# Kernel tuning notes

Measured on AMD Instinct MI355X. Metric: run time of the kernel, lower is better.

## Reference

```python
import jax, jax.numpy as jnp
import numpy as np

E = 1024   # embed_dim
H = 16     # num_heads
HD = E // H
T, B, S = 1024, 4, 1024


def setup_inputs() -> dict:
    key = jax.random.key(0)
    ks = jax.random.split(key, 6)
    g = lambda k, sh, sc=1.0: jax.random.normal(k, sh, dtype=jnp.float32) * sc
    return {
        "query": g(ks[0], (T, B, E)),
        "key": g(ks[1], (S, B, E)),
        "value": g(ks[2], (S, B, E)),
        "in_proj_weight": g(ks[3], (3 * E, E), E ** -0.5),
        "in_proj_bias": jnp.zeros((3 * E,), jnp.float32),
        "out_w": g(ks[4], (E, E), E ** -0.5),
        "out_b": jnp.zeros((E,), jnp.float32),
    }


def reference(query, key, value, in_proj_weight, in_proj_bias, out_w, out_b):
    # qkv not same and kv not same -> decorr=True cross-attention branch.
    W, b = in_proj_weight, in_proj_bias
    scaling = HD ** -0.5
    half = E // 2
    # Note: original uses F.linear(x, weight_slice.T, bias) == x @ weight_slice + bias
    q = query @ W[:E] + b[:E]                       # [T,B,E]
    k = key @ W[E:2 * E] + b[E:2 * E]               # [S,B,E]
    Wv = W[2 * E:]                                  # [E,E] V block
    v_corr = value @ Wv[:, :half] + b[2 * E:2 * E + half]      # [S,B,E/2]
    v_decorr = value @ Wv[:, half:] + b[2 * E + half:]         # [S,B,E/2]
    q = q * scaling
    # heads: [T,B,E] -> [B*H, T, hd]; per-branch V has head_dim/2 per head
    qh = q.reshape(T, B * H, HD).transpose(1, 0, 2)
    kh = k.reshape(S, B * H, HD).transpose(1, 0, 2)
    vch = v_corr.reshape(S, B * H, HD // 2).transpose(1, 0, 2)
    vdh = v_decorr.reshape(S, B * H, HD // 2).transpose(1, 0, 2)
    scores = jnp.einsum('btd,bsd->bts', qh, kh)     # [B*H, T, S]
    a_corr = jax.nn.softmax(scores, axis=-1)
    a_decorr = jax.nn.softmax(-scores, axis=-1)     # softmin(x) = softmax(-x)
    # dropout p=0.0 (eval) -> identity
    attn = jnp.concatenate([
        jnp.einsum('bts,bsd->btd', a_corr, vch),
        jnp.einsum('bts,bsd->btd', a_decorr, vdh),
    ], axis=-1)                                     # [B*H, T, HD]
    attn = attn.transpose(1, 0, 2).reshape(T, B, E)
    attn = attn @ out_w.T + out_b                   # nn.Linear out_proj
    # returned attn_weights are the RAW (pre-softmax) scores averaged over heads
    avg_w = scores.reshape(B, H, T, S).sum(axis=1) / H
    return attn, avg_w
```

## Files before the change

kernel.cpp:

```cpp
#include <hip/hip_runtime.h>
#include <hip/hip_bf16.h>


typedef __bf16 bf16;
typedef float f32x4 __attribute__((ext_vector_type(4)));
typedef float float4v __attribute__((ext_vector_type(4)));
typedef bf16 bf16x8 __attribute__((ext_vector_type(8)));
typedef bf16 bf16x4 __attribute__((ext_vector_type(4)));

#define LOG2E 1.4426950408889634f

__device__ __forceinline__ void gll16(const void* g, void* l) {
  __builtin_amdgcn_global_load_lds(
      (const __attribute__((address_space(1))) void*)g,
      (__attribute__((address_space(3))) void*)l, 16, 0, 0);
}

__device__ __forceinline__ int xcd_swz(int flat, int nwg) {
  int q = nwg >> 3;
  return (flat & 7) * q + (flat >> 3);
}

__device__ __forceinline__ bf16x4 cvt4(float4v v) {
  bf16x4 b = { (bf16)v.x, (bf16)v.y, (bf16)v.z, (bf16)v.w };
  return b;
}

__global__ __launch_bounds__(256) void prep_all(
    const float* __restrict__ W, const float* __restrict__ out_w,
    bf16* __restrict__ WT, bf16* __restrict__ owb) {
  __shared__ bf16 tile[64][72];
  int bid = blockIdx.x;
  if (bid >= 768) {
    int i = ((bid - 768) * 256 + (int)threadIdx.x) * 4;
    float4v v = *(const float4v*)(out_w + i);
    *(bf16x4*)&owb[i] = cvt4(v);
    return;
  }
  int sec = bid >> 8, bx = bid & 15, by = (bid >> 4) & 15;
  int i0 = by * 64, j0 = bx * 64;
  const float* s = W + (long)sec * 1048576;
  bf16* d = WT + (long)sec * 1048576;
  int t = threadIdx.x;
#pragma unroll
  for (int p = 0; p < 4; p++) {
    int ri = (t >> 4) + p * 16, cj = (t & 15) * 4;
    float4v vv = *(const float4v*)(s + (long)(i0 + ri) * 1024 + j0 + cj);
    *(bf16x4*)&tile[ri][cj] = cvt4(vv);
  }
  __syncthreads();
#pragma unroll
  for (int p = 0; p < 4; p++) {
    int rj = (t >> 4) + p * 16, ci = (t & 15) * 4;
    bf16x4 bv = { tile[ci][rj], tile[ci + 1][rj], tile[ci + 2][rj], tile[ci + 3][rj] };
    *(bf16x4*)&d[(long)(j0 + rj) * 1024 + i0 + ci] = bv;
  }
}

template <bool AF32>
__device__ __forceinline__ void gemm_core(
    const void* __restrict__ Av, long lda,
    const bf16* __restrict__ B, long ldb,
    void* __restrict__ C, long ldc,
    const float* __restrict__ bias, float scale, int K,
    int m0, int n0, int cmode) {
  __shared__ bf16 smem[AF32 ? 24576 : 16384];
  float* sAf = (float*)smem;
  bf16* sBb = smem + (AF32 ? 16384 : 8192);
  int t = threadIdx.x;
  int w = t >> 6, lane = t & 63, r = lane & 15, g = lane >> 4;
  int mq = (w >> 1) * 32, nq = (w & 1) * 64;
  int srow = w * 16 + (lane >> 2);
  int scol = ((lane & 3) ^ ((srow >> 1) & 3)) * 8;
  int fsw = (r >> 1) & 3;
  const bf16* Bs = B + (long)(n0 + srow) * ldb + scol;
  const bf16* As = (const bf16*)Av + (long)(m0 + srow) * lda + scol;
  int aro = lane >> 3;
  int acolf = 4 * ((lane & 7) ^ aro);
  const float* Af = (const float*)Av + (long)(m0 + w * 16 + aro) * lda + acolf;

  f32x4 acc[2][4];
#pragma unroll
  for (int mi = 0; mi < 2; mi++)
#pragma unroll
    for (int ni = 0; ni < 4; ni++) acc[mi][ni] = (f32x4){0.f, 0.f, 0.f, 0.f};

  auto stage = [&](int buf, int k) {
    if (AF32) {
      gll16(Af + k, sAf + buf * 4096 + w * 512);
      gll16(Af + 8 * lda + k, sAf + buf * 4096 + w * 512 + 256);
    } else {
      gll16(As + k, &smem[buf * 4096 + w * 512]);
    }
    gll16(Bs + k, &sBb[buf * 4096 + w * 512]);
  };
  stage(0, 0);
  __syncthreads();
  int cur = 0;
  for (int k0 = 0; k0 < K; k0 += 32) {
    if (k0 + 32 < K) stage(cur ^ 1, k0 + 32);
    bf16x8 af[2], bfr[4];
    if (AF32) {
      int rk = r & 7;
#pragma unroll
      for (int mi = 0; mi < 2; mi++) {
        int row = mq + mi * 16 + r;
        const float* pa = sAf + cur * 4096 + row * 32;
        float4v lo = *(const float4v*)(pa + 4 * ((2 * g) ^ rk));
        float4v hi = *(const float4v*)(pa + 4 * ((2 * g + 1) ^ rk));
        bf16x4 l4 = cvt4(lo), h4 = cvt4(hi);
        bf16x8 a = { l4[0], l4[1], l4[2], l4[3], h4[0], h4[1], h4[2], h4[3] };
        af[mi] = a;
      }
    } else {
#pragma unroll
      for (int mi = 0; mi < 2; mi++)
        af[mi] = *(bf16x8*)&smem[cur * 4096 + (mq + mi * 16 + r) * 32 + 8 * (g ^ fsw)];
    }
#pragma unroll
    for (int ni = 0; ni < 4; ni++)
      bfr[ni] = *(bf16x8*)&sBb[cur * 4096 + (nq + ni * 16 + r) * 32 + 8 * (g ^ fsw)];
#pragma unroll
    for (int mi = 0; mi < 2; mi++)
#pragma unroll
      for (int ni = 0; ni < 4; ni++)
        acc[mi][ni] = __builtin_amdgcn_mfma_f32_16x16x32_bf16(af[mi], bfr[ni], acc[mi][ni], 0, 0, 0);
    __syncthreads();
    cur ^= 1;
  }

  if (cmode == 2) {
#pragma unroll
    for (int mi = 0; mi < 2; mi++) {
      int tl = (mq >> 2) + mi * 4 + g;
#pragma unroll
      for (int ni = 0; ni < 4; ni++) {
        int cl = nq + ni * 16 + r;
        float bv = bias ? bias[n0 + cl] : 0.f;
        int chunkb = (nq >> 6) * 2560 + tl * 80 + ni * 16 + r;
#pragma unroll
        for (int j = 0; j < 4; j++) {
          float val = (acc[mi][ni][j] + bv) * scale;
          smem[j * 5120 + chunkb] = (bf16)val;
        }
      }
    }
    __syncthreads();
    {
      int b_ = w >> 1, hl = w & 1;
      long gbase = ((long)(b_ * 16 + (n0 >> 6) + hl)) * 65536 + (long)(m0 >> 2) * 64;
#pragma unroll
      for (int it = 0; it < 4; it++) {
        bf16x8 v = *(bf16x8*)&smem[w * 2560 + (it * 8 + (lane >> 3)) * 80 + (lane & 7) * 8];
        *(bf16x8*)&((bf16*)C)[gbase + it * 512 + lane * 8] = v;
      }
    }
    return;
  }

  if (cmode == 3) {
#pragma unroll
    for (int mi = 0; mi < 2; mi++) {
      int s32 = (mq >> 2) + mi * 4 + g;
      int gq = (s32 >> 2) & 3;
      int u = ((s32 >> 4) << 2) | (s32 & 3);
#pragma unroll
      for (int ni = 0; ni < 4; ni++) {
        int col = n0 + nq + ni * 16 + r;
        float bv = bias ? bias[col] : 0.f;
        int clbase = ((nq >> 5) + (ni >> 1)) * 2 + (ni & 1);
#pragma unroll
        for (int j = 0; j < 4; j++) {
          float val = (acc[mi][ni][j] + bv) * scale;
          smem[(j * 8 + clbase) * 512 + (gq * 16 + r) * 8 + u] = (bf16)val;
        }
      }
    }
    __syncthreads();
    int sc_ = m0 >> 7;
    int hh0 = (n0 & 511) >> 5;
    int half = n0 >> 9;
#pragma unroll
    for (int c = 0; c < 4; c++) {
      int cl = w * 4 + c;
      int b_ = cl >> 3, hl = (cl >> 1) & 3, dl = cl & 1;
      long chunk = ((long)(b_ * 16 + hh0 + hl) * 32 + sc_) * 4 + half * 2 + dl;
      bf16x8 v = *(bf16x8*)&smem[cl * 512 + lane * 8];
      *(bf16x8*)&((bf16*)C)[(chunk << 9) + lane * 8] = v;
    }
    return;
  }

#pragma unroll
  for (int mi = 0; mi < 2; mi++)
#pragma unroll
    for (int ni = 0; ni < 4; ni++) {
      int col = n0 + nq + ni * 16 + r;
      float bv = bias ? bias[col] : 0.f;
#pragma unroll
      for (int j = 0; j < 4; j++) {
        int row = m0 + mq + mi * 16 + g * 4 + j;
        float val = (acc[mi][ni][j] + bv) * scale;
        if (cmode == 1) {
          ((bf16*)C)[(long)row * ldc + col] = (bf16)val;
        } else {
          ((float*)C)[(long)row * ldc + col] = val;
        }
      }
    }
}

__global__ __launch_bounds__(512) void gemm_out(
    const bf16* __restrict__ A, const bf16* __restrict__ B,
    float* __restrict__ C, const float* __restrict__ bias) {
  int nwg = gridDim.x * gridDim.y;
  int flat = blockIdx.x + gridDim.x * blockIdx.y;
  int work = xcd_swz(flat, nwg);
  int n = work % gridDim.x, m = work / gridDim.x;
  gemm_core<false>(A, 1024, B, 1024, C, 1024, bias, 1.0f, 1024, m * 128, n * 128, 0);
}

__global__ __launch_bounds__(512) void gemm_proj(
    const float* __restrict__ q, const float* __restrict__ k,
    const float* __restrict__ v, const bf16* __restrict__ WT,
    const float* __restrict__ bias, bf16* __restrict__ qkout,
    bf16* __restrict__ vf) {
  int nwg = gridDim.x * gridDim.y * gridDim.z;
  int flat = blockIdx.x + gridDim.x * (blockIdx.y + gridDim.y * blockIdx.z);
  int work = xcd_swz(flat, nwg);
  int n = work % gridDim.x;
  int m = (work / gridDim.x) % gridDim.y;
  int z = work / (gridDim.x * gridDim.y);
  const float* A = (z == 0) ? q : ((z == 1) ? k : v);
  const bf16* B = WT + (long)z * 1048576;
  const float* bz = bias + z * 1024;
  void* C = (z == 2) ? (void*)vf : (void*)(qkout + (long)z * 4194304);
  float scale = (z == 0) ? 0.125f * LOG2E : 1.0f;
  gemm_core<true>(A, 1024, B, 1024, C, 1024, bz, scale, 1024, m * 128, n * 128,
                  z == 2 ? 3 : 2);
}

__global__ __launch_bounds__(512) void attn_avg(
    const bf16* __restrict__ qh, const bf16* __restrict__ kh,
    const bf16* __restrict__ vf, bf16* __restrict__ attn_b,
    float* __restrict__ out_avg, float avg_scale) {
  __shared__ __align__(16) bf16 smem[16384];
  int tid = threadIdx.x, w = tid >> 6, lane = tid & 63, r = lane & 15, g = lane >> 4;
  int fsw = (r >> 1) & 3;

  if (blockIdx.x >= 512) {
    bf16* sA = smem;
    bf16* sB = smem + 8192;
    int work = xcd_swz(blockIdx.x - 512, 256);
    int n0 = (work & 7) * 128;
    int m0 = ((work >> 3) & 7) * 128;
    int bb = work >> 6;
    int mq = (w >> 1) * 32, nq = (w & 1) * 64;
    int srow = w * 16 + (lane >> 2);
    int scol = ((lane & 3) ^ ((srow >> 1) & 3)) * 8;
    const bf16* As = qh + (long)bb * 1048576 + (long)(m0 + srow) * 64 + scol;
    const bf16* Bs = kh + (long)bb * 1048576 + (long)(n0 + srow) * 64 + scol;

    f32x4 acc[2][4];
#pragma unroll
    for (int mi = 0; mi < 2; mi++)
#pragma unroll
      for (int ni = 0; ni < 4; ni++) acc[mi][ni] = (f32x4){0.f, 0.f, 0.f, 0.f};

    gll16(As, &sA[w * 512]);
    gll16(Bs, &sB[w * 512]);
    __syncthreads();
    int cur = 0;
    for (int k0 = 0; k0 < 1024; k0 += 32) {
      if (k0 + 32 < 1024) {
        int kn = k0 + 32;
        long off = ((long)(kn >> 6)) * 65536 + (kn & 63);
        gll16(As + off, &sA[(cur ^ 1) * 4096 + w * 512]);
        gll16(Bs + off, &sB[(cur ^ 1) * 4096 + w * 512]);
      }
      bf16x8 af[2], bfr[4];
#pragma unroll
      for (int mi = 0; mi < 2; mi++)
        af[mi] = *(bf16x8*)&sA[cur * 4096 + (mq + mi * 16 + r) * 32 + 8 * (g ^ fsw)];
#pragma unroll
      for (int ni = 0; ni < 4; ni++)
        bfr[ni] = *(bf16x8*)&sB[cur * 4096 + (nq + ni * 16 + r) * 32 + 8 * (g ^ fsw)];
#pragma unroll
      for (int mi = 0; mi < 2; mi++)
#pragma unroll
        for (int ni = 0; ni < 4; ni++)
          acc[mi][ni] = __builtin_amdgcn_mfma_f32_16x16x32_bf16(af[mi], bfr[ni], acc[mi][ni], 0, 0, 0);
      __syncthreads();
      cur ^= 1;
    }
#pragma unroll
    for (int mi = 0; mi < 2; mi++)
#pragma unroll
      for (int ni = 0; ni < 4; ni++) {
        int col = n0 + nq + ni * 16 + r;
#pragma unroll
        for (int j = 0; j < 4; j++) {
          int row = m0 + mq + mi * 16 + g * 4 + j;
          out_avg[(long)bb * 1048576 + (long)row * 1024 + col] = acc[mi][ni][j] * avg_scale;
        }
      }
    return;
  }

  bf16* sK = smem;
  bf16* sV = smem + 8192;
  int bh = blockIdx.x & 63;
  int b = bh >> 4, h = bh & 15;
  int t0 = (blockIdx.x >> 6) * 128;
  int tw = t0 + w * 16;

  const bf16* qrow = qh + ((long)bh * 1024 + tw + r) * 64;
  bf16x8 aq0 = *(const bf16x8*)(qrow + g * 8);
  bf16x8 aq1 = *(const bf16x8*)(qrow + 32 + g * 8);

  float sp_acc = 0.f, sn_acc = 0.f;
  f32x4 o[4];
#pragma unroll
  for (int d = 0; d < 4; d++) o[d] = (f32x4){0.f, 0.f, 0.f, 0.f};

  const bf16* kbh = kh + (long)bh * 65536;
  const bf16* vbh = vf + (long)bh * 65536;

  int krow = w * 8 + (lane >> 3);
  const bf16* ksrc = kbh + (long)krow * 64 + 8 * ((lane & 7) ^ (krow & 7));
  const bf16* vsrc = vbh + w * 512 + lane * 8;
  int c0 = 8 * (g ^ (r & 7));
  int c1 = 8 * ((g + 4) ^ (r & 7));

  gll16(ksrc, &sK[w * 512]);
  gll16(vsrc, &sV[w * 512]);
  __syncthreads();
  int cur = 0;
#pragma unroll 1
  for (int st = 0; st < 16; st++) {
    if (st < 15) {
      gll16(ksrc + (st + 1) * 4096, &sK[(cur ^ 1) * 4096 + w * 512]);
      gll16(vsrc + (st + 1) * 4096, &sV[(cur ^ 1) * 4096 + w * 512]);
    }
    f32x4 sc4[4];
#pragma unroll
    for (int sf = 0; sf < 4; sf++) {
      int row = sf * 16 + r;
      bf16x8 k0 = *(const bf16x8*)&sK[cur * 4096 + row * 64 + c0];
      bf16x8 k1 = *(const bf16x8*)&sK[cur * 4096 + row * 64 + c1];
      f32x4 z = (f32x4){0.f, 0.f, 0.f, 0.f};
      z = __builtin_amdgcn_mfma_f32_16x16x32_bf16(k0, aq0, z, 0, 0, 0);
      z = __builtin_amdgcn_mfma_f32_16x16x32_bf16(k1, aq1, z, 0, 0, 0);
      sc4[sf] = z;
    }
    bf16x8 pP[2], pN[2];
#pragma unroll
    for (int sf = 0; sf < 4; sf++)
#pragma unroll
      for (int j = 0; j < 4; j++) {
        float e = __builtin_amdgcn_exp2f(sc4[sf][j]);
        sp_acc += e;
        pP[sf >> 1][(sf & 1) * 4 + j] = (bf16)e;
        float f = __builtin_amdgcn_exp2f(-sc4[sf][j]);
        sn_acc += f;
        pN[sf >> 1][(sf & 1) * 4 + j] = (bf16)f;
      }
#pragma unroll
    for (int c = 0; c < 2; c++)
#pragma unroll
      for (int dblk = 0; dblk < 4; dblk++) {
        bf16x8 vv = *(const bf16x8*)&sV[cur * 4096 + (c * 4 + dblk) * 512 + lane * 8];
        o[dblk] = __builtin_amdgcn_mfma_f32_16x16x32_bf16(
            vv, (dblk < 2) ? pP[c] : pN[c], o[dblk], 0, 0, 0);
      }
    __syncthreads();
    cur ^= 1;
  }

  sp_acc += __shfl_xor(sp_acc, 16); sp_acc += __shfl_xor(sp_acc, 32);
  sn_acc += __shfl_xor(sn_acc, 16); sn_acc += __shfl_xor(sn_acc, 32);
  float rlp = 1.f / sp_acc, rln = 1.f / sn_acc;
  long obase = ((long)(tw + r) * 4 + b) * 1024 + h * 64;
#pragma unroll
  for (int dblk = 0; dblk < 4; dblk++) {
    float rl = (dblk < 2) ? rlp : rln;
    bf16x4 ov;
#pragma unroll
    for (int j = 0; j < 4; j++) ov[j] = (bf16)(o[dblk][j] * rl);
    *(bf16x4*)&attn_b[obase + (dblk >> 1) * 32 + (dblk & 1) * 16 + g * 4] = ov;
  }
}

extern "C" void kernel_launch(void* const* d_in, const int* in_sizes, int n_in,
                              void* d_out, int out_size, void* d_ws, size_t ws_size,
                              hipStream_t stream) {
  (void)in_sizes; (void)n_in; (void)out_size; (void)ws_size;
  const float* query = (const float*)d_in[0];
  const float* key   = (const float*)d_in[1];
  const float* value = (const float*)d_in[2];
  const float* W     = (const float*)d_in[3];
  const float* bias  = (const float*)d_in[4];
  const float* out_w = (const float*)d_in[5];
  const float* out_b = (const float*)d_in[6];

  char* ws = (char*)d_ws;
  const long MB = 1 << 20;
  bf16* qh  = (bf16*)(ws + 0 * MB);
  bf16* kh  = (bf16*)(ws + 8 * MB);
  bf16* vf  = (bf16*)(ws + 24 * MB);
  bf16* ab  = (bf16*)(ws + 32 * MB);
  bf16* WT  = (bf16*)(ws + 40 * MB);
  bf16* owb = (bf16*)(ws + 46 * MB);
  float* out_attn = (float*)d_out;
  float* out_avg  = (float*)d_out + (size_t)4 * 1024 * 1024;

  prep_all<<<dim3(1792), 256, 0, stream>>>(W, out_w, WT, owb);

  gemm_proj<<<dim3(8, 32, 3), 512, 0, stream>>>(query, key, value, WT, bias, qh, vf);

  attn_avg<<<dim3(768), 512, 0, stream>>>(qh, kh, vf, ab, out_avg,
                                          1.f / (16.f * LOG2E));

  gemm_out<<<dim3(8, 32), 512, 0, stream>>>(ab, owb, out_attn, out_b);
}
```

Measured before the change: 101.8 us.

## Give out-projection GEMM a dedicated 128x64-tile kernel with double-buffered LDS

Replaces the generic gemm_core call in gemm_out with a specialised kernel that uses 128x64 tiles, 32-wide K steps, async global-to-LDS loads with double buffering, and 16x16x32 bf16 MFMAs. The grid doubles to 512 workgroups so the small 1024x4096 output GEMM fills more compute units. The unused fp32/bf16 row-store epilogue paths are removed from gemm_core. The trade is less data reuse per tile and a thin per-iteration K step with a barrier every step.

```diff
diff --git a/kernel.cpp b/kernel.cpp
--- a/kernel.cpp
+++ b/kernel.cpp
@@ -158,25 +158,25 @@
     return;
   }
 
-  if (cmode == 3) {
-#pragma unroll
-    for (int mi = 0; mi < 2; mi++) {
-      int s32 = (mq >> 2) + mi * 4 + g;
-      int gq = (s32 >> 2) & 3;
-      int u = ((s32 >> 4) << 2) | (s32 & 3);
-#pragma unroll
-      for (int ni = 0; ni < 4; ni++) {
-        int col = n0 + nq + ni * 16 + r;
-        float bv = bias ? bias[col] : 0.f;
-        int clbase = ((nq >> 5) + (ni >> 1)) * 2 + (ni & 1);
-#pragma unroll
-        for (int j = 0; j < 4; j++) {
-          float val = (acc[mi][ni][j] + bv) * scale;
-          smem[(j * 8 + clbase) * 512 + (gq * 16 + r) * 8 + u] = (bf16)val;
-        }
-      }
-    }
-    __syncthreads();
+#pragma unroll
+  for (int mi = 0; mi < 2; mi++) {
+    int s32 = (mq >> 2) + mi * 4 + g;
+    int gq = (s32 >> 2) & 3;
+    int u = ((s32 >> 4) << 2) | (s32 & 3);
+#pragma unroll
+    for (int ni = 0; ni < 4; ni++) {
+      int col = n0 + nq + ni * 16 + r;
+      float bv = bias ? bias[col] : 0.f;
+      int clbase = ((nq >> 5) + (ni >> 1)) * 2 + (ni & 1);
+#pragma unroll
+      for (int j = 0; j < 4; j++) {
+        float val = (acc[mi][ni][j] + bv) * scale;
+        smem[(j * 8 + clbase) * 512 + (gq * 16 + r) * 8 + u] = (bf16)val;
+      }
+    }
+  }
+  __syncthreads();
+  {
     int sc_ = m0 >> 7;
     int hh0 = (n0 & 511) >> 5;
     int half = n0 >> 9;
@@ -188,36 +188,71 @@
       bf16x8 v = *(bf16x8*)&smem[cl * 512 + lane * 8];
       *(bf16x8*)&((bf16*)C)[(chunk << 9) + lane * 8] = v;
     }
-    return;
-  }
-
-#pragma unroll
-  for (int mi = 0; mi < 2; mi++)
-#pragma unroll
-    for (int ni = 0; ni < 4; ni++) {
-      int col = n0 + nq + ni * 16 + r;
-      float bv = bias ? bias[col] : 0.f;
-#pragma unroll
-      for (int j = 0; j < 4; j++) {
-        int row = m0 + mq + mi * 16 + g * 4 + j;
-        float val = (acc[mi][ni][j] + bv) * scale;
-        if (cmode == 1) {
-          ((bf16*)C)[(long)row * ldc + col] = (bf16)val;
-        } else {
-          ((float*)C)[(long)row * ldc + col] = val;
-        }
-      }
-    }
+  }
 }
 
 __global__ __launch_bounds__(512) void gemm_out(
     const bf16* __restrict__ A, const bf16* __restrict__ B,
     float* __restrict__ C, const float* __restrict__ bias) {
+  __shared__ bf16 sA[2][4096];
+  __shared__ bf16 sB[2][2048];
   int nwg = gridDim.x * gridDim.y;
   int flat = blockIdx.x + gridDim.x * blockIdx.y;
   int work = xcd_swz(flat, nwg);
-  int n = work % gridDim.x, m = work / gridDim.x;
-  gemm_core<false>(A, 1024, B, 1024, C, 1024, bias, 1.0f, 1024, m * 128, n * 128, 0);
+  int n0 = (work % gridDim.x) * 64;
+  int m0 = (work / gridDim.x) * 128;
+  int t = threadIdx.x;
+  int w = t >> 6, lane = t & 63, r = lane & 15, g = lane >> 4;
+  int mq = (w >> 1) * 32, nq = (w & 1) * 32;
+  int srow = w * 16 + (lane >> 2);
+  int scol = ((lane & 3) ^ ((srow >> 1) & 3)) * 8;
+  int fsw = (r >> 1) & 3;
+  const bf16* As = A + (long)(m0 + srow) * 1024 + scol;
+  const bf16* Bs = B + (long)(n0 + srow) * 1024 + scol;
+
+  f32x4 acc[2][2];
+#pragma unroll
+  for (int mi = 0; mi < 2; mi++)
+#pragma unroll
+    for (int ni = 0; ni < 2; ni++) acc[mi][ni] = (f32x4){0.f, 0.f, 0.f, 0.f};
+
+  auto stage = [&](int buf, int k) {
+    gll16(As + k, &sA[buf][w * 512]);
+    if (w < 4) gll16(Bs + k, &sB[buf][w * 512]);
+  };
+  stage(0, 0);
+  __syncthreads();
+  int cur = 0;
+  for (int k0 = 0; k0 < 1024; k0 += 32) {
+    if (k0 + 32 < 1024) stage(cur ^ 1, k0 + 32);
+    bf16x8 af[2], bfr[2];
+#pragma unroll
+    for (int mi = 0; mi < 2; mi++)
+      af[mi] = *(bf16x8*)&sA[cur][(mq + mi * 16 + r) * 32 + 8 * (g ^ fsw)];
+#pragma unroll
+    for (int ni = 0; ni < 2; ni++)
+      bfr[ni] = *(bf16x8*)&sB[cur][(nq + ni * 16 + r) * 32 + 8 * (g ^ fsw)];
+#pragma unroll
+    for (int mi = 0; mi < 2; mi++)
+#pragma unroll
+      for (int ni = 0; ni < 2; ni++)
+        acc[mi][ni] = __builtin_amdgcn_mfma_f32_16x16x32_bf16(af[mi], bfr[ni], acc[mi][ni], 0, 0, 0);
+    __syncthreads();
+    cur ^= 1;
+  }
+
+#pragma unroll
+  for (int mi = 0; mi < 2; mi++)
+#pragma unroll
+    for (int ni = 0; ni < 2; ni++) {
+      int col = n0 + nq + ni * 16 + r;
+      float bv = bias[col];
+#pragma unroll
+      for (int j = 0; j < 4; j++) {
+        int row = m0 + mq + mi * 16 + g * 4 + j;
+        C[(long)row * 1024 + col] = acc[mi][ni][j] + bv;
+      }
+    }
 }
 
 __global__ __launch_bounds__(512) void gemm_proj(
@@ -421,5 +456,5 @@
   attn_avg<<<dim3(768), 512, 0, stream>>>(qh, kh, vf, ab, out_avg,
                                           1.f / (16.f * LOG2E));
 
-  gemm_out<<<dim3(8, 32), 512, 0, stream>>>(ab, owb, out_attn, out_b);
-}
+  gemm_out<<<dim3(16, 32), 512, 0, stream>>>(ab, owb, out_attn, out_b);
+}
```

Result: no change. 101.6 us (-0.3%).
